# Optimization experiments

Hardware: AMD Instinct MI355X
Metric: run time of the kernel (lower is better)

Reference implementation:

```python
import jax, jax.numpy as jnp
from jax import lax
import numpy as np

K = 256   # kernel_size == hidden channels (Haar basis size)
S = 16    # stride
BN_EPS = 1e-5


def _haar_matrix_unnorm(n):
    if n == 2:
        return np.array([[1.0, 1.0], [1.0, -1.0]])
    prev = _haar_matrix_unnorm(n // 2)
    top = np.kron(prev, np.array([1.0, 1.0]))
    bot = np.kron(np.eye(n // 2), np.array([1.0, -1.0]))
    return np.concatenate((top, bot))


def haar_matrix(n):
    h = _haar_matrix_unnorm(n)
    return h / np.linalg.norm(h, axis=1, keepdims=True)


def setup_inputs() -> dict:
    key = jax.random.key(0)
    ks = jax.random.split(key, 8)
    B, T = 64, 32768
    haar = jnp.asarray(haar_matrix(K), dtype=jnp.float32)          # [K, K]
    x = jax.random.normal(ks[0], (B, 1, T), dtype=jnp.float32)
    return {
        "x": x,
        # BitwiseConv1d(1, K, K, stride=S, padding=K)
        "conv_w": haar[:, None, :],                                 # [K, 1, K] (OIH)
        "conv_b": 0.01 * jax.random.normal(ks[1], (K,), dtype=jnp.float32),
        "conv_gate": jax.random.uniform(ks[2], (K, 1, K), dtype=jnp.float32),
        "conv_scale": jnp.ones((K,), dtype=jnp.float32),            # adaptive per-out-channel scale
        # BatchNorm1d(K)
        "bn_gamma": jnp.ones((K,), dtype=jnp.float32),
        "bn_beta": jnp.zeros((K,), dtype=jnp.float32),
        # BitwiseConvTranspose1d(K, 1, K, stride=S)
        "ct_w": haar.T[:, None, :],                                 # [K(in), 1(out), K] (IOH, torch layout)
        "ct_b": 0.01 * jax.random.normal(ks[3], (1,), dtype=jnp.float32),
        "ct_gate": jax.random.uniform(ks[4], (K, 1, K), dtype=jnp.float32),
        "ct_scale": jnp.ones((1,), dtype=jnp.float32),
    }


def _forward(x, conv_w, conv_b, conv_gate, conv_scale, bn_gamma, bn_beta,
             ct_w, ct_b, ct_gate, ct_scale):
    T = x.shape[2]
    # --- BitwiseConv1d: gated weights (in_bin/weight_bin = identity) ---
    # gate binarization maps gate -> (gate + 1) / 2, multiplied into weights
    w = conv_w * (conv_gate + 1.0) * 0.5                            # [K,1,K]
    h = lax.conv_general_dilated(
        x, w, window_strides=(S,), padding=[(K, K)],
        dimension_numbers=("NCH", "OIH", "NCH"))                  # [B,K,L]
    h = conv_scale[None, :, None] * (h + conv_b[None, :, None])    # adaptive scaling
    # --- ReLU then BatchNorm1d (training-mode batch statistics) ---
    h = jax.nn.relu(h)
    mu = jnp.mean(h, axis=(0, 2), keepdims=True)
    var = jnp.mean((h - mu) ** 2, axis=(0, 2), keepdims=True)
    h = (h - mu) * lax.rsqrt(var + BN_EPS)
    h = h * bn_gamma[None, :, None] + bn_beta[None, :, None]
    # --- BitwiseConvTranspose1d: gated weights, expressed as dilated conv ---
    wt = ct_w * (ct_gate + 1.0) * 0.5                               # [K_in, 1, K]
    # torch IOH -> regular-conv OIH with kernel flipped
    wr = jnp.flip(jnp.transpose(wt, (1, 0, 2)), axis=-1)            # [1, K, K]
    y = lax.conv_general_dilated(
        h, wr, window_strides=(1,), padding=[(K - 1, K - 1)],
        lhs_dilation=(S,), dimension_numbers=("NCH", "OIH", "NCH"))
    y = ct_scale[None, :, None] * (y + ct_b[None, :, None])
    # crop: out[:, :, K : T + K]
    return y[:, :, K:T + K]


def reference(x, conv_w, conv_b, conv_gate, conv_scale, bn_gamma, bn_beta,
              ct_w, ct_b, ct_gate, ct_scale):
    return _forward(x, conv_w, conv_b, conv_gate, conv_scale, bn_gamma, bn_beta,
                    ct_w, ct_b, ct_gate, ct_scale)
```

## Files before the change

kernel.cpp:

```cpp
#include <hip/hip_runtime.h>
#include <hip/hip_bf16.h>

#define BB 64
#define TT 32768
#define KK 256
#define LL 2065
#define NLT 9
#define NPART (BB*NLT)
#define NJ 19
#define HBSTR 72
#define NPT3 16

typedef __attribute__((ext_vector_type(8))) short short8;
typedef __attribute__((ext_vector_type(4))) float f32x4;
typedef __attribute__((ext_vector_type(4))) int int4v;
typedef __attribute__((ext_vector_type(2))) unsigned int uint2v;

__device__ __forceinline__ unsigned short f2bf(float f) {
    unsigned u = __builtin_bit_cast(unsigned, f);
    unsigned r = (u + 0x7FFFu + ((u >> 16) & 1u)) >> 16;
    return (unsigned short)r;
}
__device__ __forceinline__ unsigned pkbf(float a, float b) {
    unsigned r;
    asm("v_cvt_pk_bf16_f32 %0, %1, %2" : "=v"(r) : "v"(a), "v"(b));
    return r;
}
__device__ __forceinline__ void gload_lds16(const void* g, void* l) {
    __builtin_amdgcn_global_load_lds(
        (const __attribute__((address_space(1))) unsigned int*)g,
        (__attribute__((address_space(3))) unsigned int*)l, 16, 0, 0);
}

__global__ void k0_w1f(const float* __restrict__ cw, const float* __restrict__ cgt,
                       const float* __restrict__ cs, const float* __restrict__ cb,
                       unsigned short* __restrict__ W1f, float* __restrict__ cbs)
{
    int idx = blockIdx.x*256 + threadIdx.x;
    int lane = idx & 63, ntL = (idx>>6)&7, kk = (idx>>9)&7, half = idx>>12;
    int o = half*128 + ntL*16 + (lane&15);
    float sc = cs[o];
    int kbase = kk*32 + ((lane>>4)<<3);
    short8 v;
    #pragma unroll
    for (int i = 0; i < 8; ++i) {
        int gi = o*KK + kbase + i;
        v[i] = (short)f2bf(sc * cw[gi]*(cgt[gi]+1.0f)*0.5f);
    }
    *(short8*)(W1f + (size_t)idx*8) = v;
    if (blockIdx.x == 0) {
        int c = threadIdx.x;
        cbs[c] = cs[c]*cb[c];
    }
}

__global__ __launch_bounds__(256, 3)
void k1_conv(const float* __restrict__ x, const float* __restrict__ cbs,
             const unsigned short* __restrict__ W1f,
             unsigned short* __restrict__ hout,
             float* __restrict__ psum, float* __restrict__ psq)
{
    __shared__ __align__(16) char smem[13056 + 32768];
    char* xwinb = smem;
    char* wbuf  = smem + 13056;
    unsigned short* hb = (unsigned short*)smem;
    float* redS = (float*)(smem + 36864);
    float* redQ = (float*)(smem + 36864 + 4096);

    const int tid   = threadIdx.x;
    const int q     = blockIdx.x & 3;
    const int ltile = blockIdx.x >> 2;
    const int b     = blockIdx.y;
    const int l0    = ltile * 256;
    const long pos0 = (long)l0*16 - 256;
    const int lane  = tid & 63;
    const int w     = tid >> 6;

    {
        #pragma unroll
        for (int it = 0; it < 8; ++it) {
            int ci = w*8 + it;
            int kk = ci >> 2, ntl = ci & 3;
            size_t so = (size_t)((((q>>1)*8 + kk)*8 + (q&1)*4 + ntl))*1024;
            gload_lds16((const char*)W1f + so + lane*16, wbuf + ci*1024);
        }
    }
    {
        const float* xs = x + (size_t)b*TT;
        for (int g = tid; g < 272; g += 256) {
            long base = pos0 + (long)g*16;
            unsigned uu[8];
            if (base >= 0 && base + 16 <= (long)TT) {
                const float4* xv = (const float4*)(xs + base);
                float4 a0 = xv[0], a1 = xv[1], a2 = xv[2], a3 = xv[3];
                uu[0] = pkbf(a0.x, a0.y); uu[1] = pkbf(a0.z, a0.w);
                uu[2] = pkbf(a1.x, a1.y); uu[3] = pkbf(a1.z, a1.w);
                uu[4] = pkbf(a2.x, a2.y); uu[5] = pkbf(a2.z, a2.w);
                uu[6] = pkbf(a3.x, a3.y); uu[7] = pkbf(a3.z, a3.w);
            } else {
                #pragma unroll
                for (int m = 0; m < 16; m += 2) {
                    long p = base + m;
                    float f0 = (p   >= 0 && p   < TT) ? xs[p]   : 0.0f;
                    float f1 = (p+1 >= 0 && p+1 < TT) ? xs[p+1] : 0.0f;
                    uu[m>>1] = pkbf(f0, f1);
                }
            }
            int4v w0 = { (int)uu[0], (int)uu[1], (int)uu[2], (int)uu[3] };
            int4v w1 = { (int)uu[4], (int)uu[5], (int)uu[6], (int)uu[7] };
            *(int4v*)(xwinb + 48*g)      = w0;
            *(int4v*)(xwinb + 48*g + 16) = w1;
        }
    }
    __syncthreads();

    f32x4 acc[4][4];
    #pragma unroll
    for (int mt = 0; mt < 4; ++mt)
        #pragma unroll
        for (int nt = 0; nt < 4; ++nt) acc[mt][nt] = (f32x4){0.f,0.f,0.f,0.f};

    const int gq = lane >> 4;
    const int Gt = 16*gq + 16*(gq>>1);
    const int abase = 48*((w<<6) + (lane & 15)) + Gt;

    #pragma unroll
    for (int kk = 0; kk < 8; ++kk) {
        short8 bfx[4], afw[4];
        #pragma unroll
        for (int nt = 0; nt < 4; ++nt)
            bfx[nt] = *(const short8*)(xwinb + abase + nt*768 + kk*96);
        #pragma unroll
        for (int mt = 0; mt < 4; ++mt)
            afw[mt] = *(const short8*)(wbuf + (kk*4 + mt)*1024 + lane*16);
        __builtin_amdgcn_s_setprio(1);
        #pragma unroll
        for (int mt = 0; mt < 4; ++mt)
            #pragma unroll
            for (int nt = 0; nt < 4; ++nt)
                acc[mt][nt] = __builtin_amdgcn_mfma_f32_16x16x32_bf16(afw[mt], bfx[nt], acc[mt][nt], 0, 0, 0);
        __builtin_amdgcn_s_setprio(0);
    }
    __syncthreads();

    const int c0 = q*64;
    const int g  = lane >> 4;
    const int li = lane & 15;
    #pragma unroll
    for (int mt = 0; mt < 4; ++mt) {
        int cq = c0 + mt*16 + g*4;
        f32x4 cbs4 = *(const f32x4*)&cbs[cq];
        f32x4 s4 = (f32x4){0.f,0.f,0.f,0.f};
        f32x4 q4 = (f32x4){0.f,0.f,0.f,0.f};
        #pragma unroll
        for (int nt = 0; nt < 4; ++nt) {
            int lloc = (w<<6) + nt*16 + li;
            f32x4 hv;
            #pragma unroll
            for (int rr = 0; rr < 4; ++rr)
                hv[rr] = fmaxf(acc[mt][nt][rr] + cbs4[rr], 0.0f);
            uint2v pkv = { pkbf(hv[0], hv[1]), pkbf(hv[2], hv[3]) };
            *(uint2v*)(hb + lloc*HBSTR + mt*16 + g*4) = pkv;
            if (l0 + lloc < LL) { s4 += hv; q4 += hv*hv; }
        }
        #pragma unroll
        for (int d = 1; d < 4; d <<= 1) {
            #pragma unroll
            for (int rr = 0; rr < 4; ++rr) {
                s4[rr] += __shfl_xor(s4[rr], d);
                q4[rr] += __shfl_xor(q4[rr], d);
            }
        }
        if ((li & 3) == 0) {
            int slot = ((w*4 + mt)*4 + g)*4 + (li >> 2);
            *(f32x4*)&redS[slot*4] = s4;
            *(f32x4*)&redQ[slot*4] = q4;
        }
    }
    __syncthreads();

    {
        const int rsub = tid >> 3;
        const int cpos = tid & 7;
        #pragma unroll
        for (int it = 0; it < 8; ++it) {
            int row = it*32 + rsub;
            int l = l0 + row;
            if (l < LL) {
                int4v v = *(const int4v*)(hb + row*HBSTR + cpos*8);
                *(int4v*)(hout + (((size_t)(b*LL + l)) << 8) + q*64 + cpos*8) = v;
            }
        }
    }
    if (tid < 64) {
        int mt = tid >> 4, gg = (tid >> 2) & 3, rr = tid & 3;
        float s = 0.f, qq = 0.f;
        #pragma unroll
        for (int wv = 0; wv < 4; ++wv)
            #pragma unroll
            for (int l4 = 0; l4 < 4; ++l4) {
                int slot = ((wv*4 + mt)*4 + gg)*4 + l4;
                s  += redS[slot*4 + rr];
                qq += redQ[slot*4 + rr];
            }
        int c = c0 + tid;
        int slot = b*NLT + ltile;
        psum[c*NPART + slot] = s;
        psq [c*NPART + slot] = qq;
    }
}

__global__ __launch_bounds__(256)
void k2_bn(const float* __restrict__ psum, const float* __restrict__ psq,
           const float* __restrict__ bng, const float* __restrict__ bnb,
           const float* __restrict__ ctw, const float* __restrict__ ctg,
           const float* __restrict__ ctscale,
           float* __restrict__ W3s, float* __restrict__ SWS)
{
    __shared__ double rs[4], rq[4];
    __shared__ float s_a, s_bc;
    __shared__ float swl[256];
    const int c = blockIdx.x;
    const int tid = threadIdx.x;
    double s = 0.0, q = 0.0;
    for (int i = tid; i < NPART; i += 256) {
        s += (double)psum[c*NPART + i];
        q += (double)psq [c*NPART + i];
    }
    for (int off = 32; off > 0; off >>= 1) {
        s += __shfl_down(s, off);
        q += __shfl_down(q, off);
    }
    if ((tid & 63) == 0) { rs[tid >> 6] = s; rq[tid >> 6] = q; }
    __syncthreads();
    if (tid == 0) {
        double st = rs[0]+rs[1]+rs[2]+rs[3];
        double qt = rq[0]+rq[1]+rq[2]+rq[3];
        const double cnt = (double)BB * (double)LL;
        double mu = st / cnt;
        double var = qt / cnt - mu*mu;
        float rsig = (float)(1.0 / sqrt(var + 1e-5));
        float a = bng[c] * rsig;
        s_a = a;
        s_bc = bnb[c] - (float)mu * a;
    }
    __syncthreads();
    float a = s_a, bc = s_bc, scl = ctscale[0];
    int gi = c*KK + tid;
    float wt = ctw[gi] * (ctg[gi] + 1.0f) * 0.5f;
    W3s[tid*KK + c] = scl * a * wt;
    swl[tid] = wt * bc;
    __syncthreads();
    if (tid < 16) {
        float acc2 = 0.0f;
        #pragma unroll
        for (int d = 0; d < 16; ++d) acc2 += swl[d*16 + tid];
        SWS[c*16 + tid] = acc2;
    }
}

__global__ void k2b_const(const float* __restrict__ SWS, const float* __restrict__ ctb,
                          const float* __restrict__ ctscale, float* __restrict__ C2)
{
    int r = threadIdx.x;
    if (r < 16) {
        float s = 0.0f;
        for (int c = 0; c < 256; ++c) s += SWS[c*16 + r];
        C2[r] = ctscale[0] * (s + ctb[0]);
    }
}

__global__ void k2c_b2f(const float* __restrict__ W3s, unsigned short* __restrict__ B2f)
{
    int idx = blockIdx.x*256 + threadIdx.x;
    int lane = idx & 63;
    int ntG  = (idx>>6) & 3;
    int kk   = (idx>>8) & 7;
    int j    = idx>>11;
    int c    = kk*32 + ((lane>>4)<<3);
    int r    = lane & 15;
    int d    = ntG + 15 - j;
    short8 v;
    if (d >= 0 && d <= 15) {
        const float* wr = W3s + (size_t)(16*d + r)*KK + c;
        #pragma unroll
        for (int i = 0; i < 8; ++i) v[i] = (short)f2bf(wr[i]);
    } else {
        #pragma unroll
        for (int i = 0; i < 8; ++i) v[i] = 0;
    }
    *(short8*)(B2f + (size_t)idx*8) = v;
}

__global__ __launch_bounds__(512, 4)
void k3_synth(const unsigned short* __restrict__ h, const unsigned short* __restrict__ B2f,
              const float* __restrict__ C2, float* __restrict__ out)
{
    __shared__ __align__(16) char As[144*512];
    const int tid  = threadIdx.x;
    const int lane = tid & 63;
    const int w    = tid >> 6;
    const int b    = blockIdx.y;
    const int P0   = blockIdx.x * 32;

    const char* hbase = (const char*)h + (((size_t)(b*LL) + 4*P0 + 1) << 9);

    {
        const int rl = lane >> 5;
        #pragma unroll
        for (int i = 0; i < 9; ++i) {
            int r0  = w*18 + i*2;
            int row = r0 + rl;
            int chunk = (lane & 31) ^ ((row >> 2) & 7);
            gload_lds16(hbase + (size_t)row*512 + chunk*16, As + r0*512);
        }
    }
    __syncthreads();

    const int li = lane & 15;
    const int gq = lane >> 4;

    f32x4 acc[2][4];
    #pragma unroll
    for (int mt = 0; mt < 2; ++mt)
        #pragma unroll
        for (int nt = 0; nt < 4; ++nt) acc[mt][nt] = (f32x4){0.f,0.f,0.f,0.f};

    #pragma unroll 1
    for (int jj = 0; jj < 3; ++jj) {
        const int j = w + jj*8;
        if (j >= NJ) break;
        short8 bfA[4], bfB[4];
        #pragma unroll
        for (int nt = 0; nt < 4; ++nt)
            bfA[nt] = *(const short8*)(B2f + (((size_t)(j*8 + 0)*4 + nt)*64 + lane)*8);
        #pragma unroll
        for (int kk = 0; kk < 8; ++kk) {
            if (kk < 7) {
                #pragma unroll
                for (int nt = 0; nt < 4; ++nt)
                    bfB[nt] = *(const short8*)(B2f + (((size_t)(j*8 + kk+1)*4 + nt)*64 + lane)*8);
            }
            short8 af[2];
            #pragma unroll
            for (int mt = 0; mt < 2; ++mt) {
                int row = 64*mt + 4*li + j;
                int p = (kk*4 + gq) ^ ((row >> 2) & 7);
                af[mt] = *(const short8*)(As + row*512 + p*16);
            }
            __builtin_amdgcn_s_setprio(1);
            #pragma unroll
            for (int mt = 0; mt < 2; ++mt)
                #pragma unroll
                for (int nt = 0; nt < 4; ++nt)
                    acc[mt][nt] = __builtin_amdgcn_mfma_f32_16x16x32_bf16(af[mt], bfA[nt], acc[mt][nt], 0, 0, 0);
            __builtin_amdgcn_s_setprio(0);
            #pragma unroll
            for (int nt = 0; nt < 4; ++nt) bfA[nt] = bfB[nt];
        }
    }
    __syncthreads();

    float* red = (float*)As;
    #pragma unroll
    for (int mt = 0; mt < 2; ++mt)
        #pragma unroll
        for (int nt = 0; nt < 4; ++nt) {
            int u = nt*16 + li;
            #pragma unroll
            for (int rr = 0; rr < 4; ++rr) {
                int Pl = 16*mt + gq*4 + rr;
                red[w*2176 + Pl*68 + u] = acc[mt][nt][rr];
            }
        }
    __syncthreads();

    {
        int P = tid >> 4, uq = tid & 15;
        f32x4 s = (f32x4){0.f,0.f,0.f,0.f};
        #pragma unroll
        for (int c = 0; c < 8; ++c)
            s += *(const f32x4*)&red[c*2176 + P*68 + uq*4];
        int ub = (uq & 3)*4;
        f32x4 c2v = { C2[ub], C2[ub+1], C2[ub+2], C2[ub+3] };
        float* ob = out + (size_t)b*TT + (size_t)P0*64;
        *(f32x4*)&ob[P*64 + uq*4] = s + c2v;
    }
}

extern "C" void kernel_launch(void* const* d_in, const int* in_sizes, int n_in,
                              void* d_out, int out_size, void* d_ws, size_t ws_size,
                              hipStream_t stream)
{
    const float* x       = (const float*)d_in[0];
    const float* cw      = (const float*)d_in[1];
    const float* cb      = (const float*)d_in[2];
    const float* cgt     = (const float*)d_in[3];
    const float* cs      = (const float*)d_in[4];
    const float* bng     = (const float*)d_in[5];
    const float* bnb     = (const float*)d_in[6];
    const float* ctw     = (const float*)d_in[7];
    const float* ctb     = (const float*)d_in[8];
    const float* ctg     = (const float*)d_in[9];
    const float* ctscale = (const float*)d_in[10];
    float* out = (float*)d_out;

    char* ws = (char*)d_ws;
    size_t off = 0;
    unsigned short* h    = (unsigned short*)(ws + off); off += (size_t)BB*LL*KK*2;
    float* psum          = (float*)(ws + off);          off += (size_t)KK*NPART*4;
    float* psq           = (float*)(ws + off);          off += (size_t)KK*NPART*4;
    unsigned short* W1f  = (unsigned short*)(ws + off); off += 65536*2;
    float* W3s           = (float*)(ws + off);          off += (size_t)KK*KK*4;
    float* SWS           = (float*)(ws + off);          off += (size_t)KK*16*4;
    float* C2            = (float*)(ws + off);          off += 64;
    float* cbs           = (float*)(ws + off);          off += 1024;
    unsigned short* B2f  = (unsigned short*)(ws + off); off += (size_t)NJ*8*4*64*8*2;

    k0_w1f  <<<32, 256, 0, stream>>>(cw, cgt, cs, cb, W1f, cbs);
    k1_conv <<<dim3(36, BB), 256, 0, stream>>>(x, cbs, W1f, h, psum, psq);
    k2_bn   <<<KK, 256, 0, stream>>>(psum, psq, bng, bnb, ctw, ctg, ctscale, W3s, SWS);
    k2b_const<<<1, 64, 0, stream>>>(SWS, ctb, ctscale, C2);
    k2c_b2f <<<152, 256, 0, stream>>>(W3s, B2f);
    k3_synth<<<dim3(NPT3, BB), 512, 0, stream>>>(h, B2f, C2, out);
}
```

Baseline: 84.87 us.

## Pre-convert input to padded bf16 layout, parallelize const reduction, skip zero MFMA tiles

Adds a prepass kernel that converts x to bf16 once, in a padded 48-byte-stride layout, so k1_conv can fill its input window with direct global-to-LDS loads instead of converting per block with boundary branches. The C2 reduction kernel now uses 256 threads with a shared-memory tree instead of 16 serial loops. In k3_synth, B-fragment loads and MFMAs are skipped for tile indices where the banded weight block is known to be zero. The cost is an extra kernel launch plus a write and reread of a bf16 copy of x in workspace.

```diff
diff --git a/kernel.cpp b/kernel.cpp
--- a/kernel.cpp
+++ b/kernel.cpp
@@ -10,6 +10,7 @@
 #define NJ 19
 #define HBSTR 72
 #define NPT3 16
+#define XG 2336
 
 typedef __attribute__((ext_vector_type(8))) short short8;
 typedef __attribute__((ext_vector_type(4))) float f32x4;
@@ -30,6 +31,26 @@
     __builtin_amdgcn_global_load_lds(
         (const __attribute__((address_space(1))) unsigned int*)g,
         (__attribute__((address_space(3))) unsigned int*)l, 16, 0, 0);
+}
+
+__global__ void k0x_xbf(const float* __restrict__ x, unsigned short* __restrict__ xbf)
+{
+    int idx = blockIdx.x*256 + threadIdx.x;
+    int b = idx / XG, gi = idx - b*XG;
+    unsigned short* dst = xbf + (size_t)idx*24;
+    int4v w0, w1;
+    if (gi < 16 || gi > 2063) {
+        w0 = (int4v){0,0,0,0}; w1 = (int4v){0,0,0,0};
+    } else {
+        const float4* xv = (const float4*)(x + (size_t)b*TT + 16*(gi-16));
+        float4 a0 = xv[0], a1 = xv[1], a2 = xv[2], a3 = xv[3];
+        w0 = (int4v){ (int)pkbf(a0.x,a0.y), (int)pkbf(a0.z,a0.w),
+                      (int)pkbf(a1.x,a1.y), (int)pkbf(a1.z,a1.w) };
+        w1 = (int4v){ (int)pkbf(a2.x,a2.y), (int)pkbf(a2.z,a2.w),
+                      (int)pkbf(a3.x,a3.y), (int)pkbf(a3.z,a3.w) };
+    }
+    *(int4v*)dst       = w0;
+    *(int4v*)(dst + 8) = w1;
 }
 
 __global__ void k0_w1f(const float* __restrict__ cw, const float* __restrict__ cgt,
@@ -55,14 +76,14 @@
 }
 
 __global__ __launch_bounds__(256, 3)
-void k1_conv(const float* __restrict__ x, const float* __restrict__ cbs,
+void k1_conv(const unsigned short* __restrict__ xbf, const float* __restrict__ cbs,
              const unsigned short* __restrict__ W1f,
              unsigned short* __restrict__ hout,
              float* __restrict__ psum, float* __restrict__ psq)
 {
-    __shared__ __align__(16) char smem[13056 + 32768];
+    __shared__ __align__(16) char smem[13312 + 32768];
     char* xwinb = smem;
-    char* wbuf  = smem + 13056;
+    char* wbuf  = smem + 13312;
     unsigned short* hb = (unsigned short*)smem;
     float* redS = (float*)(smem + 36864);
     float* redQ = (float*)(smem + 36864 + 4096);
@@ -72,7 +93,6 @@
     const int ltile = blockIdx.x >> 2;
     const int b     = blockIdx.y;
     const int l0    = ltile * 256;
-    const long pos0 = (long)l0*16 - 256;
     const int lane  = tid & 63;
     const int w     = tid >> 6;
 
@@ -86,30 +106,12 @@
         }
     }
     {
-        const float* xs = x + (size_t)b*TT;
-        for (int g = tid; g < 272; g += 256) {
-            long base = pos0 + (long)g*16;
-            unsigned uu[8];
-            if (base >= 0 && base + 16 <= (long)TT) {
-                const float4* xv = (const float4*)(xs + base);
-                float4 a0 = xv[0], a1 = xv[1], a2 = xv[2], a3 = xv[3];
-                uu[0] = pkbf(a0.x, a0.y); uu[1] = pkbf(a0.z, a0.w);
-                uu[2] = pkbf(a1.x, a1.y); uu[3] = pkbf(a1.z, a1.w);
-                uu[4] = pkbf(a2.x, a2.y); uu[5] = pkbf(a2.z, a2.w);
-                uu[6] = pkbf(a3.x, a3.y); uu[7] = pkbf(a3.z, a3.w);
-            } else {
-                #pragma unroll
-                for (int m = 0; m < 16; m += 2) {
-                    long p = base + m;
-                    float f0 = (p   >= 0 && p   < TT) ? xs[p]   : 0.0f;
-                    float f1 = (p+1 >= 0 && p+1 < TT) ? xs[p+1] : 0.0f;
-                    uu[m>>1] = pkbf(f0, f1);
-                }
-            }
-            int4v w0 = { (int)uu[0], (int)uu[1], (int)uu[2], (int)uu[3] };
-            int4v w1 = { (int)uu[4], (int)uu[5], (int)uu[6], (int)uu[7] };
-            *(int4v*)(xwinb + 48*g)      = w0;
-            *(int4v*)(xwinb + 48*g + 16) = w1;
+        const char* xsrc = (const char*)xbf + (size_t)b*(XG*48) + (size_t)ltile*12288;
+        #pragma unroll
+        for (int it = 0; it < 4; ++it) {
+            int i = w + it*4;
+            if (i < 13)
+                gload_lds16(xsrc + i*1024 + lane*16, xwinb + i*1024);
         }
     }
     __syncthreads();
@@ -259,14 +261,23 @@
     }
 }
 
-__global__ void k2b_const(const float* __restrict__ SWS, const float* __restrict__ ctb,
-                          const float* __restrict__ ctscale, float* __restrict__ C2)
-{
-    int r = threadIdx.x;
-    if (r < 16) {
-        float s = 0.0f;
-        for (int c = 0; c < 256; ++c) s += SWS[c*16 + r];
-        C2[r] = ctscale[0] * (s + ctb[0]);
+__global__ __launch_bounds__(256)
+void k2b_const(const float* __restrict__ SWS, const float* __restrict__ ctb,
+               const float* __restrict__ ctscale, float* __restrict__ C2)
+{
+    __shared__ float accb[16][17];
+    int tid = threadIdx.x;
+    int r = tid & 15, cc = tid >> 4;
+    float s = 0.0f;
+    #pragma unroll
+    for (int i = 0; i < 16; ++i) s += SWS[(cc*16 + i)*16 + r];
+    accb[cc][r] = s;
+    __syncthreads();
+    if (tid < 16) {
+        float t = 0.0f;
+        #pragma unroll
+        for (int i = 0; i < 16; ++i) t += accb[i][tid];
+        C2[tid] = ctscale[0] * (t + ctb[0]);
     }
 }
 
@@ -333,13 +344,15 @@
         short8 bfA[4], bfB[4];
         #pragma unroll
         for (int nt = 0; nt < 4; ++nt)
-            bfA[nt] = *(const short8*)(B2f + (((size_t)(j*8 + 0)*4 + nt)*64 + lane)*8);
+            if (nt >= j-15 && nt <= j)
+                bfA[nt] = *(const short8*)(B2f + (((size_t)(j*8 + 0)*4 + nt)*64 + lane)*8);
         #pragma unroll
         for (int kk = 0; kk < 8; ++kk) {
             if (kk < 7) {
                 #pragma unroll
                 for (int nt = 0; nt < 4; ++nt)
-                    bfB[nt] = *(const short8*)(B2f + (((size_t)(j*8 + kk+1)*4 + nt)*64 + lane)*8);
+                    if (nt >= j-15 && nt <= j)
+                        bfB[nt] = *(const short8*)(B2f + (((size_t)(j*8 + kk+1)*4 + nt)*64 + lane)*8);
             }
             short8 af[2];
             #pragma unroll
@@ -353,7 +366,8 @@
             for (int mt = 0; mt < 2; ++mt)
                 #pragma unroll
                 for (int nt = 0; nt < 4; ++nt)
-                    acc[mt][nt] = __builtin_amdgcn_mfma_f32_16x16x32_bf16(af[mt], bfA[nt], acc[mt][nt], 0, 0, 0);
+                    if (nt >= j-15 && nt <= j)
+                        acc[mt][nt] = __builtin_amdgcn_mfma_f32_16x16x32_bf16(af[mt], bfA[nt], acc[mt][nt], 0, 0, 0);
             __builtin_amdgcn_s_setprio(0);
             #pragma unroll
             for (int nt = 0; nt < 4; ++nt) bfA[nt] = bfB[nt];
@@ -415,12 +429,14 @@
     float* SWS           = (float*)(ws + off);          off += (size_t)KK*16*4;
     float* C2            = (float*)(ws + off);          off += 64;
     float* cbs           = (float*)(ws + off);          off += 1024;
+    unsigned short* xbf  = (unsigned short*)(ws + off); off += (size_t)BB*XG*24*2;
     unsigned short* B2f  = (unsigned short*)(ws + off); off += (size_t)NJ*8*4*64*8*2;
 
+    k0x_xbf <<<BB*XG/256, 256, 0, stream>>>(x, xbf);
     k0_w1f  <<<32, 256, 0, stream>>>(cw, cgt, cs, cb, W1f, cbs);
-    k1_conv <<<dim3(36, BB), 256, 0, stream>>>(x, cbs, W1f, h, psum, psq);
+    k1_conv <<<dim3(36, BB), 256, 0, stream>>>(xbf, cbs, W1f, h, psum, psq);
     k2_bn   <<<KK, 256, 0, stream>>>(psum, psq, bng, bnb, ctw, ctg, ctscale, W3s, SWS);
-    k2b_const<<<1, 64, 0, stream>>>(SWS, ctb, ctscale, C2);
+    k2b_const<<<1, 256, 0, stream>>>(SWS, ctb, ctscale, C2);
     k2c_b2f <<<152, 256, 0, stream>>>(W3s, B2f);
     k3_synth<<<dim3(NPT3, BB), 512, 0, stream>>>(h, B2f, C2, out);
 }
```

Measured after the change: 86.34 us. No clear change (+1.7%).
